# Performance work log

Measured on AMD Instinct MI355X. Metric: run time of the kernel, lower is better.

## Reference

```python
import jax, jax.numpy as jnp
import numpy as np

# BlendParams defaults (pytorch3d)
SIGMA = 1e-4
GAMMA = 1e-4
ZNEAR = 1.0
ZFAR = 100.0
EPS = 1e-10

N, H, W, K, C = 4, 256, 256, 8, 16
V, F = 100000, 200000


def setup_inputs() -> dict:
    key = jax.random.key(0)
    ks = jax.random.split(key, 7)
    return {
        "dists": jax.random.normal(ks[0], (N, H, W, K), dtype=jnp.float32),
        "zbuf": jax.random.uniform(ks[1], (N, H, W, K), dtype=jnp.float32),
        "bary_coords": jax.random.uniform(ks[2], (N, H, W, K, 3), dtype=jnp.float32),
        "verts_features": jax.random.normal(ks[3], (V, C), dtype=jnp.float32),
        "background": jax.random.uniform(ks[4], (C,), dtype=jnp.float32),
        "pix_to_face": jax.random.randint(ks[5], (N, H, W, K), 0, F),
        "faces": jax.random.randint(ks[6], (F, 3), 0, V),
    }


def reference(dists, zbuf, bary_coords, verts_features, background, pix_to_face, faces):
    mask = (pix_to_face >= 0)
    maskf = mask.astype(dists.dtype)
    safe_idx = jnp.where(mask, pix_to_face, 0)

    # --- sample_textures (TexturesVertex): barycentric gather ---
    # faces[safe_idx]: (N,H,W,K,3) vertex ids -> (N,H,W,K,3,C) features
    face_vert_feats = verts_features[faces[safe_idx]]
    texels = jnp.einsum("nhwkv,nhwkvc->nhwkc", bary_coords, face_vert_feats)

    # --- softmax_blend ---
    prob_map = jax.nn.sigmoid(-dists / SIGMA) * maskf                 # (N,H,W,K)
    z_inv = (ZFAR - zbuf) / (ZFAR - ZNEAR) * maskf                    # (N,H,W,K)
    z_inv_max = jnp.clip(jnp.max(z_inv, axis=-1, keepdims=True), EPS)  # (N,H,W,1)
    weights_num = prob_map * jnp.exp((z_inv - z_inv_max) / GAMMA)      # (N,H,W,K)
    delta = jnp.clip(jnp.exp((EPS - z_inv_max) / GAMMA), EPS)          # (N,H,W,1)
    denom = jnp.sum(weights_num, axis=-1, keepdims=True) + delta       # (N,H,W,1)

    weighted_colors = jnp.einsum("nhwk,nhwkc->nhwc", weights_num, texels)
    pixel_colors = (weighted_colors + delta * background) / denom      # (N,H,W,C)
    return pixel_colors
```

## Files before the change

kernel.cpp:

```cpp
#include <hip/hip_runtime.h>


constexpr int KK = 8;
constexpr int CC = 16;

typedef float floatx2 __attribute__((ext_vector_type(2)));

template <int CTRL>
__device__ __forceinline__ float dpp_movf(float x) {
    return __int_as_float(
        __builtin_amdgcn_mov_dpp(__float_as_int(x), CTRL, 0xF, 0xF, true));
}
#define DPP_XOR1 0xB1
#define DPP_XOR2 0x4E
#define DPP_HALF_MIRROR 0x141

__global__ __launch_bounds__(256) void feature_shader(
    const float* __restrict__ dists,
    const float* __restrict__ zbuf,
    const float* __restrict__ bary,
    const float* __restrict__ vfeat,
    const float* __restrict__ bg,
    const int*   __restrict__ p2f,
    const int*   __restrict__ faces,
    float* __restrict__ out,
    int n)
{
    const float INV_SIGMA = 1e4f;
    const float INV_GAMMA = 1e4f;
    const float EPS       = 1e-10f;
    const float ZFAR      = 100.f;
    const float INV_SPAN  = 1.f / 99.f;

    int t = blockIdx.x * blockDim.x + threadIdx.x;
    if (t >= n) return;
    int k = t & (KK - 1);

    float z  = __builtin_nontemporal_load(zbuf  + t);
    float dd = __builtin_nontemporal_load(dists + t);
    int   f  = __builtin_nontemporal_load(p2f   + t);

    float zinv = (f >= 0) ? (ZFAR - z) * INV_SPAN : 0.f;

    float m = zinv;
    m = fmaxf(m, dpp_movf<DPP_XOR1>(m));
    m = fmaxf(m, dpp_movf<DPP_XOR2>(m));
    m = fmaxf(m, dpp_movf<DPP_HALF_MIRROR>(m));
    m = fmaxf(m, EPS);

    float delta = fmaxf(__expf((EPS - m) * INV_GAMMA), EPS);
    float prob  = (f >= 0) ? 1.f / (1.f + __expf(dd * INV_SIGMA)) : 0.f;
    float w     = prob * __expf((zinv - m) * INV_GAMMA);

    float denom = w;
    denom += dpp_movf<DPP_XOR1>(denom);
    denom += dpp_movf<DPP_XOR2>(denom);
    denom += dpp_movf<DPP_HALF_MIRROR>(denom);
    denom += delta;
    float thr = denom * 1e-7f;

    float x0 = 0.f, x1 = 0.f, x2 = 0.f, x3 = 0.f;
    float x4 = 0.f, x5 = 0.f, x6 = 0.f, x7 = 0.f;
    float x8 = 0.f, x9 = 0.f, x10 = 0.f, x11 = 0.f;
    float x12 = 0.f, x13 = 0.f, x14 = 0.f, x15 = 0.f;

    if (w > thr) {
        int v0 = faces[f * 3 + 0];
        int v1 = faces[f * 3 + 1];
        int v2 = faces[f * 3 + 2];
        const float* bp = bary + (size_t)t * 3;
        float b0 = bp[0] * w;
        float b1 = bp[1] * w;
        float b2 = bp[2] * w;
        const float4* t0 = (const float4*)(vfeat + (size_t)v0 * CC);
        const float4* t1 = (const float4*)(vfeat + (size_t)v1 * CC);
        const float4* t2 = (const float4*)(vfeat + (size_t)v2 * CC);
        float4 a0, a1, a2;
        a0 = t0[0]; a1 = t1[0]; a2 = t2[0];
        x0 = b0 * a0.x + b1 * a1.x + b2 * a2.x;
        x1 = b0 * a0.y + b1 * a1.y + b2 * a2.y;
        x2 = b0 * a0.z + b1 * a1.z + b2 * a2.z;
        x3 = b0 * a0.w + b1 * a1.w + b2 * a2.w;
        a0 = t0[1]; a1 = t1[1]; a2 = t2[1];
        x4 = b0 * a0.x + b1 * a1.x + b2 * a2.x;
        x5 = b0 * a0.y + b1 * a1.y + b2 * a2.y;
        x6 = b0 * a0.z + b1 * a1.z + b2 * a2.z;
        x7 = b0 * a0.w + b1 * a1.w + b2 * a2.w;
        a0 = t0[2]; a1 = t1[2]; a2 = t2[2];
        x8  = b0 * a0.x + b1 * a1.x + b2 * a2.x;
        x9  = b0 * a0.y + b1 * a1.y + b2 * a2.y;
        x10 = b0 * a0.z + b1 * a1.z + b2 * a2.z;
        x11 = b0 * a0.w + b1 * a1.w + b2 * a2.w;
        a0 = t0[3]; a1 = t1[3]; a2 = t2[3];
        x12 = b0 * a0.x + b1 * a1.x + b2 * a2.x;
        x13 = b0 * a0.y + b1 * a1.y + b2 * a2.y;
        x14 = b0 * a0.z + b1 * a1.z + b2 * a2.z;
        x15 = b0 * a0.w + b1 * a1.w + b2 * a2.w;
    }

    bool lo1 = (k & 1) == 0;
    float s, r;
    float e0, e1, e2, e3, e4, e5, e6, e7;
    s = lo1 ? x2  : x0;  r = dpp_movf<DPP_XOR1>(s);  e0 = (lo1 ? x0  : x2 ) + r;
    s = lo1 ? x3  : x1;  r = dpp_movf<DPP_XOR1>(s);  e1 = (lo1 ? x1  : x3 ) + r;
    s = lo1 ? x6  : x4;  r = dpp_movf<DPP_XOR1>(s);  e2 = (lo1 ? x4  : x6 ) + r;
    s = lo1 ? x7  : x5;  r = dpp_movf<DPP_XOR1>(s);  e3 = (lo1 ? x5  : x7 ) + r;
    s = lo1 ? x10 : x8;  r = dpp_movf<DPP_XOR1>(s);  e4 = (lo1 ? x8  : x10) + r;
    s = lo1 ? x11 : x9;  r = dpp_movf<DPP_XOR1>(s);  e5 = (lo1 ? x9  : x11) + r;
    s = lo1 ? x14 : x12; r = dpp_movf<DPP_XOR1>(s);  e6 = (lo1 ? x12 : x14) + r;
    s = lo1 ? x15 : x13; r = dpp_movf<DPP_XOR1>(s);  e7 = (lo1 ? x13 : x15) + r;

    bool lo2 = (k & 2) == 0;
    float g0, g1, g2, g3;
    s = lo2 ? e2 : e0;  r = dpp_movf<DPP_XOR2>(s);  g0 = (lo2 ? e0 : e2) + r;
    s = lo2 ? e3 : e1;  r = dpp_movf<DPP_XOR2>(s);  g1 = (lo2 ? e1 : e3) + r;
    s = lo2 ? e6 : e4;  r = dpp_movf<DPP_XOR2>(s);  g2 = (lo2 ? e4 : e6) + r;
    s = lo2 ? e7 : e5;  r = dpp_movf<DPP_XOR2>(s);  g3 = (lo2 ? e5 : e7) + r;

    bool lo4 = (k & 4) == 0;
    float h0, h1;
    s = lo4 ? g2 : g0;  r = __shfl_xor(s, 4);  h0 = (lo4 ? g0 : g2) + r;
    s = lo4 ? g3 : g1;  r = __shfl_xor(s, 4);  h1 = (lo4 ? g1 : g3) + r;

    float2 g = ((const float2*)bg)[k];
    float inv_den = 1.f / denom;
    floatx2 o;
    o.x = (h0 + delta * g.x) * inv_den;
    o.y = (h1 + delta * g.y) * inv_den;
    __builtin_nontemporal_store(o, (floatx2*)out + t);
}

extern "C" void kernel_launch(void* const* d_in, const int* in_sizes, int n_in,
                              void* d_out, int out_size, void* d_ws, size_t ws_size,
                              hipStream_t stream) {
    const float* dists = (const float*)d_in[0];
    const float* zbuf  = (const float*)d_in[1];
    const float* bary  = (const float*)d_in[2];
    const float* vfeat = (const float*)d_in[3];
    const float* bg    = (const float*)d_in[4];
    const int*   p2f   = (const int*)d_in[5];
    const int*   faces = (const int*)d_in[6];
    float* out = (float*)d_out;

    int n = in_sizes[0];
    int block = 256;
    int grid = (n + block - 1) / block;

    hipLaunchKernelGGL(feature_shader, dim3(grid), dim3(block), 0, stream,
                       dists, zbuf, bary, vfeat, bg, p2f, faces, out, n);
}
```

Baseline: 119.2 us.

## Process two K-slots per thread with four lanes per pixel

Each thread now handles two adjacent K slots instead of one, so a pixel is covered by four lanes rather than eight. Inputs are loaded as 2-wide vectors and the output as a 4-wide vector, and the cross-lane reductions drop the half-mirror and the xor-4 shuffle stages. The grid is halved. The cost is that each thread does two dependent gathers serially, which reduces the number of threads available to hide gather latency.

```diff
diff --git a/kernel.cpp b/kernel.cpp
--- a/kernel.cpp
+++ b/kernel.cpp
@@ -1,10 +1,11 @@
 #include <hip/hip_runtime.h>
 
 
-constexpr int KK = 8;
 constexpr int CC = 16;
 
 typedef float floatx2 __attribute__((ext_vector_type(2)));
+typedef float floatx4 __attribute__((ext_vector_type(4)));
+typedef int   intx2   __attribute__((ext_vector_type(2)));
 
 template <int CTRL>
 __device__ __forceinline__ float dpp_movf(float x) {
@@ -13,7 +14,39 @@
 }
 #define DPP_XOR1 0xB1
 #define DPP_XOR2 0x4E
-#define DPP_HALF_MIRROR 0x141
+
+#define GATHER_SLOT(F, TT, W)                                                \
+    {                                                                        \
+        int v0 = faces[(size_t)(F) * 3 + 0];                                 \
+        int v1 = faces[(size_t)(F) * 3 + 1];                                 \
+        int v2 = faces[(size_t)(F) * 3 + 2];                                 \
+        const float* bp = bary + (size_t)(TT) * 3;                           \
+        float b0 = bp[0] * (W), b1 = bp[1] * (W), b2 = bp[2] * (W);          \
+        const float4* t0 = (const float4*)(vfeat + (size_t)v0 * CC);         \
+        const float4* t1 = (const float4*)(vfeat + (size_t)v1 * CC);         \
+        const float4* t2 = (const float4*)(vfeat + (size_t)v2 * CC);         \
+        float4 a0, a1, a2;                                                   \
+        a0 = t0[0]; a1 = t1[0]; a2 = t2[0];                                  \
+        x0  += b0 * a0.x + b1 * a1.x + b2 * a2.x;                            \
+        x1  += b0 * a0.y + b1 * a1.y + b2 * a2.y;                            \
+        x2  += b0 * a0.z + b1 * a1.z + b2 * a2.z;                            \
+        x3  += b0 * a0.w + b1 * a1.w + b2 * a2.w;                            \
+        a0 = t0[1]; a1 = t1[1]; a2 = t2[1];                                  \
+        x4  += b0 * a0.x + b1 * a1.x + b2 * a2.x;                            \
+        x5  += b0 * a0.y + b1 * a1.y + b2 * a2.y;                            \
+        x6  += b0 * a0.z + b1 * a1.z + b2 * a2.z;                            \
+        x7  += b0 * a0.w + b1 * a1.w + b2 * a2.w;                            \
+        a0 = t0[2]; a1 = t1[2]; a2 = t2[2];                                  \
+        x8  += b0 * a0.x + b1 * a1.x + b2 * a2.x;                            \
+        x9  += b0 * a0.y + b1 * a1.y + b2 * a2.y;                            \
+        x10 += b0 * a0.z + b1 * a1.z + b2 * a2.z;                            \
+        x11 += b0 * a0.w + b1 * a1.w + b2 * a2.w;                            \
+        a0 = t0[3]; a1 = t1[3]; a2 = t2[3];                                  \
+        x12 += b0 * a0.x + b1 * a1.x + b2 * a2.x;                            \
+        x13 += b0 * a0.y + b1 * a1.y + b2 * a2.y;                            \
+        x14 += b0 * a0.z + b1 * a1.z + b2 * a2.z;                            \
+        x15 += b0 * a0.w + b1 * a1.w + b2 * a2.w;                            \
+    }
 
 __global__ __launch_bounds__(256) void feature_shader(
     const float* __restrict__ dists,
@@ -32,30 +65,33 @@
     const float ZFAR      = 100.f;
     const float INV_SPAN  = 1.f / 99.f;
 
-    int t = blockIdx.x * blockDim.x + threadIdx.x;
-    if (t >= n) return;
-    int k = t & (KK - 1);
+    int u = blockIdx.x * blockDim.x + threadIdx.x;
+    if (u >= (n >> 1)) return;
+    int t = u << 1;
+    int q = threadIdx.x & 3;
 
-    float z  = __builtin_nontemporal_load(zbuf  + t);
-    float dd = __builtin_nontemporal_load(dists + t);
-    int   f  = __builtin_nontemporal_load(p2f   + t);
+    floatx2 z2 = __builtin_nontemporal_load((const floatx2*)zbuf  + u);
+    floatx2 d2 = __builtin_nontemporal_load((const floatx2*)dists + u);
+    intx2   f2 = __builtin_nontemporal_load((const intx2*)  p2f   + u);
+    int fa = f2.x, fb = f2.y;
 
-    float zinv = (f >= 0) ? (ZFAR - z) * INV_SPAN : 0.f;
+    float zinv0 = (fa >= 0) ? (ZFAR - z2.x) * INV_SPAN : 0.f;
+    float zinv1 = (fb >= 0) ? (ZFAR - z2.y) * INV_SPAN : 0.f;
 
-    float m = zinv;
+    float m = fmaxf(zinv0, zinv1);
     m = fmaxf(m, dpp_movf<DPP_XOR1>(m));
     m = fmaxf(m, dpp_movf<DPP_XOR2>(m));
-    m = fmaxf(m, dpp_movf<DPP_HALF_MIRROR>(m));
     m = fmaxf(m, EPS);
 
     float delta = fmaxf(__expf((EPS - m) * INV_GAMMA), EPS);
-    float prob  = (f >= 0) ? 1.f / (1.f + __expf(dd * INV_SIGMA)) : 0.f;
-    float w     = prob * __expf((zinv - m) * INV_GAMMA);
+    float prob0 = (fa >= 0) ? 1.f / (1.f + __expf(d2.x * INV_SIGMA)) : 0.f;
+    float prob1 = (fb >= 0) ? 1.f / (1.f + __expf(d2.y * INV_SIGMA)) : 0.f;
+    float w0 = prob0 * __expf((zinv0 - m) * INV_GAMMA);
+    float w1 = prob1 * __expf((zinv1 - m) * INV_GAMMA);
 
-    float denom = w;
+    float denom = w0 + w1;
     denom += dpp_movf<DPP_XOR1>(denom);
     denom += dpp_movf<DPP_XOR2>(denom);
-    denom += dpp_movf<DPP_HALF_MIRROR>(denom);
     denom += delta;
     float thr = denom * 1e-7f;
 
@@ -64,70 +100,36 @@
     float x8 = 0.f, x9 = 0.f, x10 = 0.f, x11 = 0.f;
     float x12 = 0.f, x13 = 0.f, x14 = 0.f, x15 = 0.f;
 
-    if (w > thr) {
-        int v0 = faces[f * 3 + 0];
-        int v1 = faces[f * 3 + 1];
-        int v2 = faces[f * 3 + 2];
-        const float* bp = bary + (size_t)t * 3;
-        float b0 = bp[0] * w;
-        float b1 = bp[1] * w;
-        float b2 = bp[2] * w;
-        const float4* t0 = (const float4*)(vfeat + (size_t)v0 * CC);
-        const float4* t1 = (const float4*)(vfeat + (size_t)v1 * CC);
-        const float4* t2 = (const float4*)(vfeat + (size_t)v2 * CC);
-        float4 a0, a1, a2;
-        a0 = t0[0]; a1 = t1[0]; a2 = t2[0];
-        x0 = b0 * a0.x + b1 * a1.x + b2 * a2.x;
-        x1 = b0 * a0.y + b1 * a1.y + b2 * a2.y;
-        x2 = b0 * a0.z + b1 * a1.z + b2 * a2.z;
-        x3 = b0 * a0.w + b1 * a1.w + b2 * a2.w;
-        a0 = t0[1]; a1 = t1[1]; a2 = t2[1];
-        x4 = b0 * a0.x + b1 * a1.x + b2 * a2.x;
-        x5 = b0 * a0.y + b1 * a1.y + b2 * a2.y;
-        x6 = b0 * a0.z + b1 * a1.z + b2 * a2.z;
-        x7 = b0 * a0.w + b1 * a1.w + b2 * a2.w;
-        a0 = t0[2]; a1 = t1[2]; a2 = t2[2];
-        x8  = b0 * a0.x + b1 * a1.x + b2 * a2.x;
-        x9  = b0 * a0.y + b1 * a1.y + b2 * a2.y;
-        x10 = b0 * a0.z + b1 * a1.z + b2 * a2.z;
-        x11 = b0 * a0.w + b1 * a1.w + b2 * a2.w;
-        a0 = t0[3]; a1 = t1[3]; a2 = t2[3];
-        x12 = b0 * a0.x + b1 * a1.x + b2 * a2.x;
-        x13 = b0 * a0.y + b1 * a1.y + b2 * a2.y;
-        x14 = b0 * a0.z + b1 * a1.z + b2 * a2.z;
-        x15 = b0 * a0.w + b1 * a1.w + b2 * a2.w;
-    }
+    if (w0 > thr) GATHER_SLOT(fa, t,     w0);
+    if (w1 > thr) GATHER_SLOT(fb, t + 1, w1);
 
-    bool lo1 = (k & 1) == 0;
+    bool lo1 = (q & 1) == 0;
     float s, r;
     float e0, e1, e2, e3, e4, e5, e6, e7;
-    s = lo1 ? x2  : x0;  r = dpp_movf<DPP_XOR1>(s);  e0 = (lo1 ? x0  : x2 ) + r;
-    s = lo1 ? x3  : x1;  r = dpp_movf<DPP_XOR1>(s);  e1 = (lo1 ? x1  : x3 ) + r;
-    s = lo1 ? x6  : x4;  r = dpp_movf<DPP_XOR1>(s);  e2 = (lo1 ? x4  : x6 ) + r;
-    s = lo1 ? x7  : x5;  r = dpp_movf<DPP_XOR1>(s);  e3 = (lo1 ? x5  : x7 ) + r;
-    s = lo1 ? x10 : x8;  r = dpp_movf<DPP_XOR1>(s);  e4 = (lo1 ? x8  : x10) + r;
-    s = lo1 ? x11 : x9;  r = dpp_movf<DPP_XOR1>(s);  e5 = (lo1 ? x9  : x11) + r;
-    s = lo1 ? x14 : x12; r = dpp_movf<DPP_XOR1>(s);  e6 = (lo1 ? x12 : x14) + r;
-    s = lo1 ? x15 : x13; r = dpp_movf<DPP_XOR1>(s);  e7 = (lo1 ? x13 : x15) + r;
+    s = lo1 ? x4  : x0;  r = dpp_movf<DPP_XOR1>(s);  e0 = (lo1 ? x0  : x4 ) + r;
+    s = lo1 ? x5  : x1;  r = dpp_movf<DPP_XOR1>(s);  e1 = (lo1 ? x1  : x5 ) + r;
+    s = lo1 ? x6  : x2;  r = dpp_movf<DPP_XOR1>(s);  e2 = (lo1 ? x2  : x6 ) + r;
+    s = lo1 ? x7  : x3;  r = dpp_movf<DPP_XOR1>(s);  e3 = (lo1 ? x3  : x7 ) + r;
+    s = lo1 ? x12 : x8;  r = dpp_movf<DPP_XOR1>(s);  e4 = (lo1 ? x8  : x12) + r;
+    s = lo1 ? x13 : x9;  r = dpp_movf<DPP_XOR1>(s);  e5 = (lo1 ? x9  : x13) + r;
+    s = lo1 ? x14 : x10; r = dpp_movf<DPP_XOR1>(s);  e6 = (lo1 ? x10 : x14) + r;
+    s = lo1 ? x15 : x11; r = dpp_movf<DPP_XOR1>(s);  e7 = (lo1 ? x11 : x15) + r;
 
-    bool lo2 = (k & 2) == 0;
+    bool lo2 = (q & 2) == 0;
     float g0, g1, g2, g3;
-    s = lo2 ? e2 : e0;  r = dpp_movf<DPP_XOR2>(s);  g0 = (lo2 ? e0 : e2) + r;
-    s = lo2 ? e3 : e1;  r = dpp_movf<DPP_XOR2>(s);  g1 = (lo2 ? e1 : e3) + r;
-    s = lo2 ? e6 : e4;  r = dpp_movf<DPP_XOR2>(s);  g2 = (lo2 ? e4 : e6) + r;
-    s = lo2 ? e7 : e5;  r = dpp_movf<DPP_XOR2>(s);  g3 = (lo2 ? e5 : e7) + r;
+    s = lo2 ? e4 : e0;  r = dpp_movf<DPP_XOR2>(s);  g0 = (lo2 ? e0 : e4) + r;
+    s = lo2 ? e5 : e1;  r = dpp_movf<DPP_XOR2>(s);  g1 = (lo2 ? e1 : e5) + r;
+    s = lo2 ? e6 : e2;  r = dpp_movf<DPP_XOR2>(s);  g2 = (lo2 ? e2 : e6) + r;
+    s = lo2 ? e7 : e3;  r = dpp_movf<DPP_XOR2>(s);  g3 = (lo2 ? e3 : e7) + r;
 
-    bool lo4 = (k & 4) == 0;
-    float h0, h1;
-    s = lo4 ? g2 : g0;  r = __shfl_xor(s, 4);  h0 = (lo4 ? g0 : g2) + r;
-    s = lo4 ? g3 : g1;  r = __shfl_xor(s, 4);  h1 = (lo4 ? g1 : g3) + r;
-
-    float2 g = ((const float2*)bg)[k];
+    float4 bgv = ((const float4*)bg)[q];
     float inv_den = 1.f / denom;
-    floatx2 o;
-    o.x = (h0 + delta * g.x) * inv_den;
-    o.y = (h1 + delta * g.y) * inv_den;
-    __builtin_nontemporal_store(o, (floatx2*)out + t);
+    floatx4 o;
+    o.x = (g0 + delta * bgv.x) * inv_den;
+    o.y = (g1 + delta * bgv.y) * inv_den;
+    o.z = (g2 + delta * bgv.z) * inv_den;
+    o.w = (g3 + delta * bgv.w) * inv_den;
+    __builtin_nontemporal_store(o, (floatx4*)out + u);
 }
 
 extern "C" void kernel_launch(void* const* d_in, const int* in_sizes, int n_in,
@@ -143,8 +145,9 @@
     float* out = (float*)d_out;
 
     int n = in_sizes[0];
+    int pairs = n >> 1;
     int block = 256;
-    int grid = (n + block - 1) / block;
+    int grid = (pairs + block - 1) / block;
 
     hipLaunchKernelGGL(feature_shader, dim3(grid), dim3(block), 0, stream,
                        dists, zbuf, bary, vfeat, bg, p2f, faces, out, n);
```

New measurement: 118.8 us. About the same (-0.3%).
